# Kernel optimization log

Measured on AMD Instinct MI355X. Metric: run time of the kernel, lower is better.

## Reference

```python
import jax, jax.numpy as jnp
import numpy as np

DIM = 1024
HEADS = 16


def setup_inputs() -> dict:
    key = jax.random.key(0)
    k1, k2, k3, k4 = jax.random.split(key, 4)
    X = jax.random.normal(k1, (4, 2048, DIM), dtype=jnp.float32)
    # torch Linear weight is [out, in]; store transposed [in, out] for x @ W
    W_qkv = jax.random.normal(k2, (DIM, 3 * DIM), dtype=jnp.float32) * (DIM ** -0.5)
    W_out = jax.random.normal(k3, (DIM, DIM), dtype=jnp.float32) * (DIM ** -0.5)
    b_out = jax.random.normal(k4, (DIM,), dtype=jnp.float32) * 0.01
    return {"X": X, "W_qkv": W_qkv, "W_out": W_out, "b_out": b_out}


def reference(X, W_qkv, W_out, b_out):
    b, t, d = X.shape
    h = HEADS
    hd = d // h
    scale = d ** -0.5  # NOTE: scales by full dim, matching the original module
    qkv = X @ W_qkv  # [b, t, 3d]
    q, k, v = jnp.split(qkv, 3, axis=-1)
    # [b, t, d] -> [b, h, t, hd]
    def to_heads(x):
        return x.reshape(b, t, h, hd).transpose(0, 2, 1, 3)
    q, k, v = to_heads(q), to_heads(k), to_heads(v)
    dots = jnp.einsum('bhid,bhjd->bhij', q, k) * scale  # [b, h, t, t]
    attn = jax.nn.softmax(dots, axis=-1)
    out = jnp.einsum('bhij,bhjd->bhid', attn, v)  # [b, h, t, hd]
    out = out.transpose(0, 2, 1, 3).reshape(b, t, d)
    return out @ W_out + b_out
```

## Files before the change

### kernel.cpp

```cpp
#include <hip/hip_runtime.h>
#include <hip/hip_bf16.h>
#include <stdint.h>

#define DIMD 1024
#define NB 4
#define NT 2048
#define NH 16
#define BT (NB*NT)
#define NQKV (3*DIMD)

typedef __attribute__((ext_vector_type(8))) __bf16 bf16x8;
typedef __attribute__((ext_vector_type(4))) __bf16 bf16x4;
typedef __attribute__((ext_vector_type(4))) float f32x4;
typedef __attribute__((ext_vector_type(16))) float f32x16;

#define MFMA16(a,b,c) __builtin_amdgcn_mfma_f32_16x16x32_bf16((a),(b),(c),0,0,0)
#define MFMA32(a,b,c) __builtin_amdgcn_mfma_f32_32x32x16_bf16((a),(b),(c),0,0,0)

#define QSCALE 0.0450842200277801f

__device__ __forceinline__ void gld16(const void* g, void* l) {
  __builtin_amdgcn_global_load_lds((const __attribute__((address_space(1))) void*)g,
                                   (__attribute__((address_space(3))) void*)l,
                                   16, 0, 0);
}

__device__ __forceinline__ unsigned pkbf(float a, float b) {
  unsigned short ua = __builtin_bit_cast(unsigned short, (__bf16)a);
  unsigned short ub = __builtin_bit_cast(unsigned short, (__bf16)b);
  return (unsigned)ua | ((unsigned)ub << 16);
}

__global__ __launch_bounds__(256) void k_cvt(const float* __restrict__ in,
                                             __bf16* __restrict__ out, int n4) {
  int i = blockIdx.x * blockDim.x + threadIdx.x;
  int st = gridDim.x * blockDim.x;
  for (; i < n4; i += st) {
    float4 v = ((const float4*)in)[i];
    bf16x4 o;
    o[0] = (__bf16)v.x; o[1] = (__bf16)v.y; o[2] = (__bf16)v.z; o[3] = (__bf16)v.w;
    ((bf16x4*)out)[i] = o;
  }
}

__global__ __launch_bounds__(256) void k_tcvt(const float* __restrict__ in,
                                              __bf16* __restrict__ out, int K, int N) {
  __shared__ __bf16 t[64][72];
  int n0 = blockIdx.x * 64, k0 = blockIdx.y * 64;
  int r = threadIdx.x >> 2, c0 = (threadIdx.x & 3) * 16;
  const float4* src = (const float4*)(in + (size_t)(k0 + r) * N + n0 + c0);
#pragma unroll
  for (int i = 0; i < 4; ++i) {
    float4 v = src[i];
    t[r][c0 + i*4 + 0] = (__bf16)v.x;
    t[r][c0 + i*4 + 1] = (__bf16)v.y;
    t[r][c0 + i*4 + 2] = (__bf16)v.z;
    t[r][c0 + i*4 + 3] = (__bf16)v.w;
  }
  __syncthreads();
  bf16x8 o0, o1;
#pragma unroll
  for (int i = 0; i < 8; ++i) o0[i] = t[c0 + i][r];
#pragma unroll
  for (int i = 0; i < 8; ++i) o1[i] = t[c0 + 8 + i][r];
  __bf16* dst = out + (size_t)(n0 + r) * K + k0 + c0;
  *(bf16x8*)dst = o0;
  *(bf16x8*)(dst + 8) = o1;
}

template<int MODE>
__global__ __launch_bounds__(512, 1) void k_gemm256(const __bf16* __restrict__ A,
                                                    const __bf16* __restrict__ Bt,
                                                    int nbx,
                                                    __bf16* __restrict__ oQK,
                                                    __bf16* __restrict__ oVt,
                                                    float* __restrict__ oF,
                                                    const float* __restrict__ bias) {
  constexpr int KK = 1024, KT = 32;
  __shared__ alignas(16) char L[98304];
  const int tid = threadIdx.x;
  const int lane = tid & 63, wid = tid >> 6;
  const int lr = lane & 15, lo = lane >> 4;
  const int wm = wid >> 2, wn = wid & 3;
  const int cpx = gridDim.x >> 3;
  const int swz = (blockIdx.x & 7) * cpx + (blockIdx.x >> 3);
  const int bx = swz % nbx, by = swz / nbx;
  const int m0 = by * 128, n0 = bx * 256;

  const int srow = tid >> 2, sk = (tid & 3) * 8;
  const __bf16* Asr = A + (size_t)(m0 + srow) * KK + sk;
  const __bf16* Bs0 = Bt + (size_t)(n0 + srow) * KK + sk;
  const __bf16* Bs1 = Bt + (size_t)(n0 + 128 + srow) * KK + sk;

  auto STAGE = [&](int t) {
    const int s = t & 3;
    char* dA = L + s * 8192 + tid * 16;
    char* dB = L + 32768 + s * 16384 + tid * 16;
    gld16(Asr + t * 32, dA);
    gld16(Bs0 + t * 32, dB);
    gld16(Bs1 + t * 32, dB + 8192);
  };

  const __bf16* fA = (const __bf16*)L + (size_t)(wm * 64 + lr) * 32 + lo * 8;
  const __bf16* fB = (const __bf16*)(L + 32768) + (size_t)(wn * 64 + lr) * 32 + lo * 8;

  f32x4 acc[4][4] = {};
  STAGE(0); STAGE(1); STAGE(2);

  for (int t = 0; t < KT; ++t) {
    if (t < KT - 2)       asm volatile("s_waitcnt vmcnt(6)" ::: "memory");
    else if (t == KT - 2) asm volatile("s_waitcnt vmcnt(3)" ::: "memory");
    else                  asm volatile("s_waitcnt vmcnt(0)" ::: "memory");
    asm volatile("s_barrier" ::: "memory");
    if (t + 3 < KT) STAGE(t + 3);
    const __bf16* fa = fA + (t & 3) * 4096;
    const __bf16* fb = fB + (t & 3) * 8192;
    bf16x8 Af[4], Bf[4];
#pragma unroll
    for (int i = 0; i < 4; ++i) Af[i] = *(const bf16x8*)(fa + i * 512);
#pragma unroll
    for (int j = 0; j < 4; ++j) Bf[j] = *(const bf16x8*)(fb + j * 512);
    __builtin_amdgcn_s_setprio(1);
#pragma unroll
    for (int i = 0; i < 4; ++i)
#pragma unroll
      for (int j = 0; j < 4; ++j)
        acc[i][j] = MFMA16(Af[i], Bf[j], acc[i][j]);
    __builtin_amdgcn_s_setprio(0);
  }

  const int mb = m0 + wm * 64 + lo * 4;
  if (MODE == 0) {
    if (n0 < 1024) {
#pragma unroll
      for (int i = 0; i < 4; ++i)
#pragma unroll
        for (int j = 0; j < 4; ++j) {
          int col = n0 + wn * 64 + j * 16 + lr;
          int row = mb + i * 16;
#pragma unroll
          for (int r = 0; r < 4; ++r)
            oQK[(size_t)(row + r) * 2048 + col] = (__bf16)(acc[i][j][r] * QSCALE);
        }
    } else if (n0 < 2048) {
#pragma unroll
      for (int i = 0; i < 4; ++i)
#pragma unroll
        for (int j = 0; j < 4; ++j) {
          int col = n0 + wn * 64 + j * 16 + lr;
          int row = mb + i * 16;
#pragma unroll
          for (int r = 0; r < 4; ++r)
            oQK[(size_t)(row + r) * 2048 + col] = (__bf16)acc[i][j][r];
        }
    } else {
#pragma unroll
      for (int i = 0; i < 4; ++i)
#pragma unroll
        for (int j = 0; j < 4; ++j) {
          int dd = n0 - 2048 + wn * 64 + j * 16 + lr;
          int row = mb + i * 16;
          int bb = row >> 11, tt = row & 2047;
          bf16x4 pk;
#pragma unroll
          for (int r = 0; r < 4; ++r) pk[r] = (__bf16)acc[i][j][r];
          *(bf16x4*)(oVt + ((size_t)(bb << 10) + dd) * 2048 + tt) = pk;
        }
    }
  } else {
#pragma unroll
    for (int i = 0; i < 4; ++i)
#pragma unroll
      for (int j = 0; j < 4; ++j) {
        int col = n0 + wn * 64 + j * 16 + lr;
        float bv = bias[col];
        int row = mb + i * 16;
#pragma unroll
        for (int r = 0; r < 4; ++r)
          oF[(size_t)(row + r) * 1024 + col] = acc[i][j][r] + bv;
      }
  }
}

__global__ __launch_bounds__(256, 2) void k_attn(const __bf16* __restrict__ QK,
                                                 const __bf16* __restrict__ Vt,
                                                 __bf16* __restrict__ AO) {
  __shared__ alignas(16) char Lsm[3 * 18432];
  const int tid = threadIdx.x, w = tid >> 6, lane = tid & 63;
  const int l31 = lane & 31, hi = lane >> 5;
  const int P = blockIdx.x;
  const int low3 = P & 7, g = P >> 3;
  const int qc = g & 7;
  const int bh = ((g >> 3) << 3) + low3;
  const int h = bh & 15, b = bh >> 4;
  const int q0 = qc * 256 + w * 64;

  bf16x8 qfA[4], qfB[4];
  {
    const __bf16* Qb = QK + (size_t)(b * 2048 + q0 + l31) * 2048 + h * 64 + hi * 8;
#pragma unroll
    for (int dc = 0; dc < 4; ++dc) qfA[dc] = *(const bf16x8*)(Qb + dc * 16);
    Qb += (size_t)32 * 2048;
#pragma unroll
    for (int dc = 0; dc < 4; ++dc) qfB[dc] = *(const bf16x8*)(Qb + dc * 16);
  }
  const __bf16* Kg = QK + (size_t)(b * 2048) * 2048 + 1024 + h * 64;
  const __bf16* Vg = Vt + (size_t)(b * 1024 + h * 64) * 2048;

  const bool nch5 = (tid < 128);
  const char* gp[5];
  int loff[5], advB[5];
#pragma unroll
  for (int j = 0; j < 5; ++j) {
    int c = (j < 4) ? (j * 256 + tid) : (1024 + tid);
    if (c > 1151) c = 1151;
    int isV = (c >= 576);
    int lc = isV ? c - 576 : c;
    int row = lc / 9, col = lc - row * 9; if (col == 8) col = 0;
    const __bf16* gsrc = isV ? (Vg + (size_t)row * 2048 + col * 8)
                             : (Kg + (size_t)row * 2048 + col * 8);
    gp[j] = (const char*)gsrc;
    loff[j] = c * 16;
    advB[j] = isV ? 128 : 262144;
  }

  f32x16 oA0 = {0,0,0,0,0,0,0,0,0,0,0,0,0,0,0,0};
  f32x16 oA1 = {0,0,0,0,0,0,0,0,0,0,0,0,0,0,0,0};
  f32x16 oB0 = {0,0,0,0,0,0,0,0,0,0,0,0,0,0,0,0};
  f32x16 oB1 = {0,0,0,0,0,0,0,0,0,0,0,0,0,0,0,0};
  float lnA = 0.f, lnB = 0.f;

  auto STAGE = [&](int s) {
    char* bas = Lsm + s * 18432;
    gld16(gp[0], bas + loff[0]); gp[0] += advB[0];
    gld16(gp[1], bas + loff[1]); gp[1] += advB[1];
    gld16(gp[2], bas + loff[2]); gp[2] += advB[2];
    gld16(gp[3], bas + loff[3]); gp[3] += advB[3];
    if (nch5) { gld16(gp[4], bas + loff[4]); gp[4] += advB[4]; }
  };

  auto SMPACK = [&](const f32x16& s0, const f32x16& s1, unsigned pw[4][4], float& ln) {
    float p0a[16], p1a[16];
#pragma unroll
    for (int r = 0; r < 16; ++r) {
      p0a[r] = __builtin_amdgcn_exp2f(s0[r]);
      p1a[r] = __builtin_amdgcn_exp2f(s1[r]);
    }
    float sA = 0.f, sB = 0.f, sC = 0.f, sD = 0.f;
#pragma unroll
    for (int r = 0; r < 4; ++r) {
      sA += p0a[r];      sB += p0a[4 + r];
      sC += p0a[8 + r];  sD += p0a[12 + r];
      sA += p1a[r];      sB += p1a[4 + r];
      sC += p1a[8 + r];  sD += p1a[12 + r];
    }
    ln += (sA + sB) + (sC + sD);
#pragma unroll
    for (int c = 0; c < 4; ++c) {
      const float* pp = (c < 2) ? p0a : p1a;
      const int rb = (c & 1) * 8;
      unsigned A01 = pkbf(pp[rb + 0], pp[rb + 1]);
      unsigned A23 = pkbf(pp[rb + 2], pp[rb + 3]);
      unsigned A45 = pkbf(pp[rb + 4], pp[rb + 5]);
      unsigned A67 = pkbf(pp[rb + 6], pp[rb + 7]);
      asm("v_permlane32_swap_b32 %0, %1" : "+v"(A01), "+v"(A45));
      asm("v_permlane32_swap_b32 %0, %1" : "+v"(A23), "+v"(A67));
      pw[c][0] = A01; pw[c][1] = A23; pw[c][2] = A45; pw[c][3] = A67;
    }
  };

  STAGE(0); STAGE(1);
  int xc = 0, xs = 2;

  for (int t = 0; t < 32; ++t) {
    if (t == 31)   asm volatile("s_waitcnt vmcnt(0)" ::: "memory");
    else if (nch5) asm volatile("s_waitcnt vmcnt(5)" ::: "memory");
    else           asm volatile("s_waitcnt vmcnt(4)" ::: "memory");
    __builtin_amdgcn_s_barrier();
    if (t <= 29) { STAGE(xs); xs = (xs == 2) ? 0 : xs + 1; }

    const __bf16* Kl = (const __bf16*)(Lsm + xc * 18432);
    const __bf16* Vl = Kl + 4608;

    f32x16 sA0 = {0,0,0,0,0,0,0,0,0,0,0,0,0,0,0,0};
    f32x16 sA1 = {0,0,0,0,0,0,0,0,0,0,0,0,0,0,0,0};
    f32x16 sB0 = {0,0,0,0,0,0,0,0,0,0,0,0,0,0,0,0};
    f32x16 sB1 = {0,0,0,0,0,0,0,0,0,0,0,0,0,0,0,0};
    {
      bf16x8 kf[8];
#pragma unroll
      for (int dc = 0; dc < 4; ++dc)
        kf[dc] = *(const bf16x8*)(Kl + l31 * 72 + dc * 16 + hi * 8);
#pragma unroll
      for (int dc = 0; dc < 4; ++dc)
        kf[4 + dc] = *(const bf16x8*)(Kl + (32 + l31) * 72 + dc * 16 + hi * 8);
      __builtin_amdgcn_s_setprio(1);
#pragma unroll
      for (int dc = 0; dc < 4; ++dc) {
        sA0 = MFMA32(kf[dc], qfA[dc], sA0);
        sB0 = MFMA32(kf[dc], qfB[dc], sB0);
        sA1 = MFMA32(kf[4 + dc], qfA[dc], sA1);
        sB1 = MFMA32(kf[4 + dc], qfB[dc], sB1);
      }
      __builtin_amdgcn_s_setprio(0);
    }

    unsigned pwA[4][4], pwB[4][4];
    SMPACK(sA0, sA1, pwA, lnA);
    SMPACK(sB0, sB1, pwB, lnB);

    {
      bf16x8 vf[8];
#pragma unroll
      for (int c = 0; c < 4; ++c)
        vf[c] = *(const bf16x8*)(Vl + l31 * 72 + c * 16 + hi * 8);
#pragma unroll
      for (int c = 0; c < 4; ++c)
        vf[4 + c] = *(const bf16x8*)(Vl + (32 + l31) * 72 + c * 16 + hi * 8);
      __builtin_amdgcn_s_setprio(1);
#pragma unroll
      for (int c = 0; c < 4; ++c) {
        union { unsigned u[4]; bf16x8 v; } pa, pb;
        pa.u[0] = pwA[c][0]; pa.u[1] = pwA[c][1]; pa.u[2] = pwA[c][2]; pa.u[3] = pwA[c][3];
        pb.u[0] = pwB[c][0]; pb.u[1] = pwB[c][1]; pb.u[2] = pwB[c][2]; pb.u[3] = pwB[c][3];
        oA0 = MFMA32(pa.v, vf[c], oA0);
        oB0 = MFMA32(pb.v, vf[c], oB0);
        oA1 = MFMA32(pa.v, vf[4 + c], oA1);
        oB1 = MFMA32(pb.v, vf[4 + c], oB1);
      }
      __builtin_amdgcn_s_setprio(0);
    }

    xc = (xc == 2) ? 0 : xc + 1;
  }

  float lA = lnA + __shfl_xor(lnA, 32, 64);
  float lB = lnB + __shfl_xor(lnB, 32, 64);
  float invA = 1.0f / lA, invB = 1.0f / lB;
  __bf16* Ob = AO + (size_t)(b * 2048 + q0) * 1024 + h * 64;
#pragma unroll
  for (int r = 0; r < 16; ++r) {
    int qr = (r & 3) + 8 * (r >> 2) + 4 * hi;
    float ivA = __shfl(invA, qr, 64);
    float ivB = __shfl(invB, qr, 64);
    Ob[(size_t)qr * 1024 + l31] = (__bf16)(oA0[r] * ivA);
    Ob[(size_t)qr * 1024 + 32 + l31] = (__bf16)(oA1[r] * ivA);
    Ob[(size_t)(32 + qr) * 1024 + l31] = (__bf16)(oB0[r] * ivB);
    Ob[(size_t)(32 + qr) * 1024 + 32 + l31] = (__bf16)(oB1[r] * ivB);
  }
}

extern "C" void kernel_launch(void* const* d_in, const int* in_sizes, int n_in,
                              void* d_out, int out_size, void* d_ws, size_t ws_size,
                              hipStream_t stream) {
  const float* X    = (const float*)d_in[0];
  const float* Wqkv = (const float*)d_in[1];
  const float* Wout = (const float*)d_in[2];
  const float* bout = (const float*)d_in[3];
  float* out = (float*)d_out;
  char* ws = (char*)d_ws;

  __bf16* Xb  = (__bf16*)(ws);
  __bf16* Wqt = (__bf16*)(ws + 16777216);
  __bf16* Wot = (__bf16*)(ws + 23068672);
  __bf16* QKb = (__bf16*)(ws + 25165824);
  __bf16* Vtb = (__bf16*)(ws + 58720256);
  __bf16* AOb = (__bf16*)(ws + 75497472);

  k_cvt<<<2048, 256, 0, stream>>>(X, Xb, (BT * DIMD) / 4);
  k_tcvt<<<dim3(NQKV / 64, DIMD / 64), 256, 0, stream>>>(Wqkv, Wqt, DIMD, NQKV);
  k_tcvt<<<dim3(DIMD / 64, DIMD / 64), 256, 0, stream>>>(Wout, Wot, DIMD, DIMD);
  k_gemm256<0><<<768, 512, 0, stream>>>(Xb, Wqt, 12, QKb, Vtb, nullptr, nullptr);
  k_attn<<<512, 256, 0, stream>>>(QKb, Vtb, AOb);
  k_gemm256<1><<<256, 512, 0, stream>>>(AOb, Wot, 4, nullptr, nullptr, out, bout);
}
```

Baseline: 199.0 us.

## Shrink GEMM tiles to 128x128 with 4 waves and a three-stage LDS pipeline

The GEMM kernels now use 128x128 output tiles computed by 256 threads (four waves in a 2x2 arrangement) instead of 128x256 tiles with 512 threads. The LDS ring drops from four stages to three and uses a unified 16KB stage layout, and launch bounds now allow three blocks per CU. The grids double so the QKV and output projections get more blocks and better occupancy and load balance. In exchange, each block reuses A and B less, so total global and L2 traffic rises.

```diff
diff --git a/kernel.cpp b/kernel.cpp
--- a/kernel.cpp
+++ b/kernel.cpp
@@ -69,7 +69,7 @@
 }
 
 template<int MODE>
-__global__ __launch_bounds__(512, 1) void k_gemm256(const __bf16* __restrict__ A,
+__global__ __launch_bounds__(256, 3) void k_gemm128(const __bf16* __restrict__ A,
                                                     const __bf16* __restrict__ Bt,
                                                     int nbx,
                                                     __bf16* __restrict__ oQK,
@@ -77,44 +77,48 @@
                                                     float* __restrict__ oF,
                                                     const float* __restrict__ bias) {
   constexpr int KK = 1024, KT = 32;
-  __shared__ alignas(16) char L[98304];
+  __shared__ alignas(16) char L[3 * 16384];
   const int tid = threadIdx.x;
   const int lane = tid & 63, wid = tid >> 6;
   const int lr = lane & 15, lo = lane >> 4;
-  const int wm = wid >> 2, wn = wid & 3;
+  const int wm = wid >> 1, wn = wid & 1;
   const int cpx = gridDim.x >> 3;
   const int swz = (blockIdx.x & 7) * cpx + (blockIdx.x >> 3);
   const int bx = swz % nbx, by = swz / nbx;
-  const int m0 = by * 128, n0 = bx * 256;
-
-  const int srow = tid >> 2, sk = (tid & 3) * 8;
-  const __bf16* Asr = A + (size_t)(m0 + srow) * KK + sk;
-  const __bf16* Bs0 = Bt + (size_t)(n0 + srow) * KK + sk;
-  const __bf16* Bs1 = Bt + (size_t)(n0 + 128 + srow) * KK + sk;
-
-  auto STAGE = [&](int t) {
-    const int s = t & 3;
-    char* dA = L + s * 8192 + tid * 16;
-    char* dB = L + 32768 + s * 16384 + tid * 16;
-    gld16(Asr + t * 32, dA);
-    gld16(Bs0 + t * 32, dB);
-    gld16(Bs1 + t * 32, dB + 8192);
+  const int m0 = by * 128, n0 = bx * 128;
+
+  const char* gp[4];
+  int loff[4];
+#pragma unroll
+  for (int j = 0; j < 4; ++j) {
+    int c = j * 256 + tid;
+    int isB = (c >= 512);
+    int lc = c & 511;
+    int row = lc >> 2, kof = (lc & 3) * 8;
+    const __bf16* base = isB ? (Bt + (size_t)(n0 + row) * KK + kof)
+                             : (A + (size_t)(m0 + row) * KK + kof);
+    gp[j] = (const char*)base;
+    loff[j] = c * 16;
+  }
+  auto STAGE = [&](int s) {
+    char* bas = L + s * 16384;
+    gld16(gp[0], bas + loff[0]); gp[0] += 64;
+    gld16(gp[1], bas + loff[1]); gp[1] += 64;
+    gld16(gp[2], bas + loff[2]); gp[2] += 64;
+    gld16(gp[3], bas + loff[3]); gp[3] += 64;
   };
 
-  const __bf16* fA = (const __bf16*)L + (size_t)(wm * 64 + lr) * 32 + lo * 8;
-  const __bf16* fB = (const __bf16*)(L + 32768) + (size_t)(wn * 64 + lr) * 32 + lo * 8;
-
   f32x4 acc[4][4] = {};
-  STAGE(0); STAGE(1); STAGE(2);
+  STAGE(0); STAGE(1);
+  int xs = 2;
 
   for (int t = 0; t < KT; ++t) {
-    if (t < KT - 2)       asm volatile("s_waitcnt vmcnt(6)" ::: "memory");
-    else if (t == KT - 2) asm volatile("s_waitcnt vmcnt(3)" ::: "memory");
-    else                  asm volatile("s_waitcnt vmcnt(0)" ::: "memory");
+    if (t == KT - 1) asm volatile("s_waitcnt vmcnt(0)" ::: "memory");
+    else             asm volatile("s_waitcnt vmcnt(4)" ::: "memory");
     asm volatile("s_barrier" ::: "memory");
-    if (t + 3 < KT) STAGE(t + 3);
-    const __bf16* fa = fA + (t & 3) * 4096;
-    const __bf16* fb = fB + (t & 3) * 8192;
+    if (t <= KT - 3) { STAGE(xs); xs = (xs == 2) ? 0 : xs + 1; }
+    const __bf16* fa = (const __bf16*)(L + (t % 3) * 16384) + (wm * 64 + lr) * 32 + lo * 8;
+    const __bf16* fb = (const __bf16*)(L + (t % 3) * 16384 + 8192) + (wn * 64 + lr) * 32 + lo * 8;
     bf16x8 Af[4], Bf[4];
 #pragma unroll
     for (int i = 0; i < 4; ++i) Af[i] = *(const bf16x8*)(fa + i * 512);
@@ -370,7 +374,7 @@
   k_cvt<<<2048, 256, 0, stream>>>(X, Xb, (BT * DIMD) / 4);
   k_tcvt<<<dim3(NQKV / 64, DIMD / 64), 256, 0, stream>>>(Wqkv, Wqt, DIMD, NQKV);
   k_tcvt<<<dim3(DIMD / 64, DIMD / 64), 256, 0, stream>>>(Wout, Wot, DIMD, DIMD);
-  k_gemm256<0><<<768, 512, 0, stream>>>(Xb, Wqt, 12, QKb, Vtb, nullptr, nullptr);
+  k_gemm128<0><<<1536, 256, 0, stream>>>(Xb, Wqt, 24, QKb, Vtb, nullptr, nullptr);
   k_attn<<<512, 256, 0, stream>>>(QKb, Vtb, AOb);
-  k_gemm256<1><<<256, 512, 0, stream>>>(AOb, Wot, 4, nullptr, nullptr, out, bout);
-}
+  k_gemm128<1><<<512, 256, 0, stream>>>(AOb, Wot, 8, nullptr, nullptr, out, bout);
+}
```

Result: faster. 187.4 us (-5.8%).
